# Kernel tuning notes

Hardware: AMD Instinct MI355X
Metric: run time of the kernel (lower is better)

Reference implementation:

```python
import jax, jax.numpy as jnp
import numpy as np

EMB = 2048
HD = 64            # head_dim
NH = 32            # n_heads
NKV = 8            # n_kv_groups
GS = NH // NKV     # group_size = 4
WIN = 128          # sliding_window
LAYER_IDX = 0      # even -> sliding-window mask active
ROPE_BASE = 10000.0
MAX_SEQ = 4096
YARN_ORIG = 1024.0
YARN_SCALE = 4.0
YARN_BETA_FAST = 32.0
YARN_BETA_SLOW = 1.0


def _rope_tables():
    # YaRN-adjusted RoPE tables, shape [MAX_SEQ, HD]
    freqs = 1.0 / ROPE_BASE ** (np.arange(0, HD, 2, dtype=np.float32) / HD)
    wave_len = 2.0 * np.pi / freqs
    low = YARN_ORIG / YARN_BETA_FAST
    high = YARN_ORIG / YARN_BETA_SLOW
    t = np.clip((wave_len - low) / (high - low), 0.0, 1.0)
    eff = freqs * (1.0 - t) + (freqs / YARN_SCALE) * t
    conc = 0.1 * np.log(YARN_SCALE) + 1.0
    ang = (np.arange(MAX_SEQ, dtype=np.float32)[:, None] * eff[None, :]) * conc
    ang = np.concatenate([ang, ang], axis=-1).astype(np.float32)
    return jnp.sin(ang), jnp.cos(ang)


def _apply_rope(x, sin, cos):
    # x: [B, H, S, D]; sin/cos: [B, S, D] -> broadcast over heads
    sin = sin[:, None, :, :]
    cos = cos[:, None, :, :]
    x1 = x[..., : HD // 2]
    x2 = x[..., HD // 2 :]
    rotated = jnp.concatenate([-x2, x1], axis=-1)
    return x * cos + rotated * sin


def setup_inputs() -> dict:
    key = jax.random.key(0)
    ks = jax.random.split(key, 8)
    B, S = 2, 2048
    s = 0.02
    x = jax.random.normal(ks[0], (B, S, EMB), dtype=jnp.float32)
    Wq = jax.random.normal(ks[1], (NH * HD, EMB), dtype=jnp.float32) * s
    Wk = jax.random.normal(ks[2], (NKV * HD, EMB), dtype=jnp.float32) * s
    Wv = jax.random.normal(ks[3], (NKV * HD, EMB), dtype=jnp.float32) * s
    Wo = jax.random.normal(ks[4], (EMB, NH * HD), dtype=jnp.float32) * s
    bq = jnp.zeros((NH * HD,), dtype=jnp.float32)
    bk = jnp.zeros((NKV * HD,), dtype=jnp.float32)
    bv = jnp.zeros((NKV * HD,), dtype=jnp.float32)
    bo = jnp.zeros((EMB,), dtype=jnp.float32)
    sinks = jax.random.normal(ks[5], (1, NH, 1, 1), dtype=jnp.float32)
    position_ids = jnp.arange(B * S, dtype=jnp.int64 if jax.config.jax_enable_x64 else jnp.int32).reshape(B, S)
    return {"x": x, "Wq": Wq, "bq": bq, "Wk": Wk, "bk": bk, "Wv": Wv, "bv": bv,
            "Wo": Wo, "bo": bo, "sinks": sinks, "position_ids": position_ids}


def reference(x, Wq, bq, Wk, bk, Wv, bv, Wo, bo, sinks, position_ids):
    B, S, _ = x.shape
    sin_t, cos_t = _rope_tables()
    sin = sin_t[position_ids]  # [B, S, HD]
    cos = cos_t[position_ids]

    Q = (x @ Wq.T + bq).reshape(B, S, NH, HD).transpose(0, 2, 1, 3)    # [B,NH,S,D]
    K = (x @ Wk.T + bk).reshape(B, S, NKV, HD).transpose(0, 2, 1, 3)   # [B,NKV,S,D]
    V = (x @ Wv.T + bv).reshape(B, S, NKV, HD).transpose(0, 2, 1, 3)

    Q = _apply_rope(Q, sin, cos)
    K = _apply_rope(K, sin, cos)

    # GQA without materializing repeated K/V: group query heads by kv group
    Qg = Q.reshape(B, NKV, GS, S, HD)
    scores = jnp.einsum('bgqsd,bgtd->bgqst', Qg, K) / np.sqrt(HD).astype(np.float32)

    i = jnp.arange(S)[:, None]
    j = jnp.arange(S)[None, :]
    allowed = (j <= i) & (j > i - WIN)
    scores = jnp.where(allowed, scores, -jnp.inf)

    # attention-sink logit prepended before softmax, then dropped
    sink = jnp.broadcast_to(sinks.reshape(1, NKV, GS, 1, 1), (B, NKV, GS, S, 1))
    full = jnp.concatenate([sink, scores], axis=-1)
    attn = jax.nn.softmax(full, axis=-1)[..., 1:]

    ctx = jnp.einsum('bgqst,bgtd->bgqsd', attn, V)
    ctx = ctx.reshape(B, NH, S, HD).transpose(0, 2, 1, 3).reshape(B, S, NH * HD)
    out = ctx @ Wo.T + bo
    return out
```

## Files before the change

kernel.cpp:

```cpp
#include <hip/hip_runtime.h>

typedef unsigned short u16;
typedef __bf16 bf16x8 __attribute__((ext_vector_type(8)));
typedef float f32x4 __attribute__((ext_vector_type(4)));
typedef unsigned short us8 __attribute__((ext_vector_type(8)));

__device__ inline u16 f2bf(float f) {
    union { float f; unsigned u; } v; v.f = f;
    unsigned r = v.u + 0x7FFFu + ((v.u >> 16) & 1u);
    return (u16)(r >> 16);
}
__device__ inline float bf2f(u16 h) {
    union { unsigned u; float f; } v; v.u = ((unsigned)h) << 16;
    return v.f;
}
__device__ inline f32x4 mfma16(bf16x8 a, bf16x8 b, f32x4 c) {
    return __builtin_amdgcn_mfma_f32_16x16x32_bf16(a, b, c, 0, 0, 0);
}
__device__ inline void gload_lds16(const u16* g, u16* l) {
    __builtin_amdgcn_global_load_lds(
        (const __attribute__((address_space(1))) void*)g,
        (__attribute__((address_space(3))) void*)l, 16, 0, 0);
}
union frag_cast { us8 u; bf16x8 b; };

__global__ __launch_bounds__(256)
void pack_all(const float* __restrict__ x,  const float* __restrict__ Wq,
              const float* __restrict__ Wk, const float* __restrict__ Wv,
              const float* __restrict__ Wo, const float* __restrict__ bq,
              const float* __restrict__ bk, const float* __restrict__ bv,
              u16* __restrict__ xb, u16* __restrict__ Wqkvb,
              u16* __restrict__ Wob, float* __restrict__ bqkv,
              float2* __restrict__ tab)
{
    int blk = blockIdx.x;
    if (blk >= 9217) {
        int idx = (blk - 9217) * 256 + threadIdx.x;
        int d = idx & 31, pos = idx >> 5;
        float ex = (float)d * (1.0f / 32.0f);
        float freq = powf(10000.0f, -ex);
        float wl = 6.2831853071795864f / freq;
        float tt = fminf(fmaxf((wl - 32.0f) * (1.0f / 992.0f), 0.0f), 1.0f);
        float eff = (freq * (1.0f - tt) + 0.25f * freq * tt) * 1.1386294361119891f;
        float ang = (float)pos * eff;
        tab[idx] = make_float2(cosf(ang), sinf(ang));
        return;
    }
    if (blk == 9216) {
        for (int k = threadIdx.x; k < 3072; k += 256) {
            float v;
            if (k < 2048) v = bq[k];
            else if (k < 2560) v = bk[k - 2048];
            else v = bv[k - 2560];
            bqkv[k] = v;
        }
        return;
    }
    const float* src; u16* dst; size_t off;
    if (blk < 4096)      { src = x;  dst = xb;                 off = (size_t)blk * 2048; }
    else if (blk < 6144) { src = Wq; dst = Wqkvb;              off = (size_t)(blk - 4096) * 2048; }
    else if (blk < 6656) { src = Wk; dst = Wqkvb + 4194304;    off = (size_t)(blk - 6144) * 2048; }
    else if (blk < 7168) { src = Wv; dst = Wqkvb + 5242880;    off = (size_t)(blk - 6656) * 2048; }
    else                 { src = Wo; dst = Wob;                off = (size_t)(blk - 7168) * 2048; }
    size_t i = off + (size_t)threadIdx.x * 8;
    float4 v0 = *(const float4*)(src + i);
    float4 v1 = *(const float4*)(src + i + 4);
    us8 w;
    w[0] = f2bf(v0.x); w[1] = f2bf(v0.y); w[2] = f2bf(v0.z); w[3] = f2bf(v0.w);
    w[4] = f2bf(v1.x); w[5] = f2bf(v1.y); w[6] = f2bf(v1.z); w[7] = f2bf(v1.w);
    *(us8*)(dst + i) = w;
}

template<int NBX, int OUT_BF16>
__global__ __launch_bounds__(256, 3)
void gemm_128(const u16* __restrict__ A, const u16* __restrict__ B,
              const float* __restrict__ bias, void* __restrict__ Yv,
              int M, int N, int K)
{
    __shared__ u16 lds[3 * 8192];

    const int tid = threadIdx.x;
    const int lane = tid & 63;
    const int w = tid >> 6;
    const int wr = w >> 1, wc = w & 1;
    const int wg = blockIdx.x;
    const int cpx = (NBX * 32) >> 3;
    const int swz = (wg & 7) * cpx + (wg >> 3);
    const int by = swz / NBX, bx = swz - by * NBX;
    const long m0 = (long)by * 128;
    const long n0 = (long)bx * 128;
    const int cc = lane & 15, qq = lane >> 4;
    const int csw = (qq ^ ((cc >> 1) & 3)) << 3;

    const int sr = lane >> 2;
    const int colsw = ((lane & 3) ^ ((lane >> 3) & 3)) << 3;
    const u16* gA0 = A + (m0 + w * 16 + sr) * (long)K + colsw;
    const u16* gA1 = gA0 + 64 * (long)K;
    const u16* gB0 = B + (n0 + w * 16 + sr) * (long)K + colsw;
    const u16* gB1 = gB0 + 64 * (long)K;

    const int NT = K >> 5;

    auto STAGE = [&](int k0, int bi) {
        u16* buf = &lds[bi * 8192];
        gload_lds16(gA0 + k0, buf + w * 512);
        gload_lds16(gA1 + k0, buf + (4 + w) * 512);
        gload_lds16(gB0 + k0, buf + (8 + w) * 512);
        gload_lds16(gB1 + k0, buf + (12 + w) * 512);
    };

    f32x4 acc[4][4];
#pragma unroll
    for (int i = 0; i < 4; i++)
#pragma unroll
        for (int j = 0; j < 4; j++) acc[i][j] = (f32x4){0.f, 0.f, 0.f, 0.f};

    STAGE(0, 0);
    int bR = 0;
    for (int t = 0; t < NT; ++t) {
        int bW = bR + 1; if (bW == 3) bW = 0;
        if (t + 1 < NT) {
            STAGE((t + 1) << 5, bW);
            asm volatile("s_waitcnt vmcnt(4)" ::: "memory");
        } else {
            asm volatile("s_waitcnt vmcnt(0)" ::: "memory");
        }
        __builtin_amdgcn_s_barrier();
        __builtin_amdgcn_sched_barrier(0);

        const u16* Ab = &lds[bR * 8192];
        bf16x8 af[4], bfr[4];
#pragma unroll
        for (int j = 0; j < 4; ++j)
            bfr[j] = *(const bf16x8*)&Ab[4096 + (wc * 64 + j * 16 + cc) * 32 + csw];
#pragma unroll
        for (int i = 0; i < 4; ++i)
            af[i] = *(const bf16x8*)&Ab[(wr * 64 + i * 16 + cc) * 32 + csw];

        __builtin_amdgcn_s_setprio(1);
#pragma unroll
        for (int i = 0; i < 4; ++i)
#pragma unroll
            for (int j = 0; j < 4; ++j)
                acc[i][j] = mfma16(af[i], bfr[j], acc[i][j]);
        __builtin_amdgcn_s_setprio(0);
        bR = bW;
    }

#pragma unroll
    for (int i = 0; i < 4; ++i) {
#pragma unroll
        for (int j = 0; j < 4; ++j) {
            long row = m0 + wr * 64 + i * 16 + qq * 4;
            long col = n0 + wc * 64 + j * 16 + cc;
            float bvv = bias[col];
#pragma unroll
            for (int r2 = 0; r2 < 4; ++r2) {
                float v = acc[i][j][r2] + bvv;
                if (OUT_BF16)
                    ((u16*)Yv)[(row + r2) * (long)N + col] = f2bf(v);
                else
                    ((float*)Yv)[(row + r2) * (long)N + col] = v;
            }
        }
    }
}

__global__ __launch_bounds__(256)
void v_transpose(const u16* __restrict__ Vt, u16* __restrict__ VbT)
{
    __shared__ u16 tile[64][66];
    int s0 = blockIdx.x * 64;
    int bkv = blockIdx.y;
    int b = bkv >> 3, kv = bkv & 7;
    int t = threadIdx.x;
#pragma unroll
    for (int it = 0; it < 16; ++it) {
        int idx = t + it * 256;
        int s = idx >> 6, d = idx & 63;
        tile[s][d] = Vt[((size_t)(b * 2048 + s0 + s)) * 3072 + 2560 + kv * 64 + d];
    }
    __syncthreads();
#pragma unroll
    for (int it = 0; it < 16; ++it) {
        int idx = t + it * 256;
        int d = idx >> 6, s = idx & 63;
        VbT[((size_t)(bkv * 64 + d)) * 2048 + s0 + s] = tile[s][d];
    }
}

__global__ __launch_bounds__(256, 2)
void attn_win2(const u16* __restrict__ QKVr, const u16* __restrict__ VbT,
               const float2* __restrict__ tab, const int* __restrict__ pid,
               const float* __restrict__ sinks, u16* __restrict__ Ctx)
{
    __shared__ u16 Ks[192 * 72];
    __shared__ u16 Vs[64 * 200];
    __shared__ u16 Pb[4 * 16 * 200];
    const int S = 2048;
    const int tid = threadIdx.x;
    const int lane = tid & 63;
    const int w = tid >> 6;
    const int cc = lane & 15, qq = lane >> 4;
    const int blk = blockIdx.x;
    const int qt = blk & 31;
    const int bkv = blk >> 5;
    const int b = bkv >> 3, kv = bkv & 7;
    const int q0 = qt * 64;
    const int ks0 = q0 - 128;
    const int h = kv * 4 + w;

    {
        const int kcol = 2048 + kv * 64;
#pragma unroll
        for (int it = 0; it < 3; ++it) {
            int c = tid + it * 256;
            int kk = c >> 2, dlo = (c & 3) << 3;
            int sk = ks0 + kk;
            us8 lo = {0, 0, 0, 0, 0, 0, 0, 0};
            us8 hi = {0, 0, 0, 0, 0, 0, 0, 0};
            if (sk >= 0) {
                size_t rowoff = (size_t)(b * S + sk) * 3072 + kcol;
                us8 li = *(const us8*)(QKVr + rowoff + dlo);
                us8 hiQ = *(const us8*)(QKVr + rowoff + dlo + 32);
                int pos = pid[b * S + sk];
                const float2* tp = tab + pos * 32 + dlo;
#pragma unroll
                for (int jj = 0; jj < 8; ++jj) {
                    float2 cs = tp[jj];
                    float x1 = bf2f(li[jj]), x2 = bf2f(hiQ[jj]);
                    lo[jj] = f2bf(x1 * cs.x - x2 * cs.y);
                    hi[jj] = f2bf(x2 * cs.x + x1 * cs.y);
                }
            }
            *(us8*)&Ks[kk * 72 + dlo] = lo;
            *(us8*)&Ks[kk * 72 + dlo + 32] = hi;
        }
    }
    const u16* VtBase = VbT + (size_t)bkv * 64 * S;
#pragma unroll
    for (int it = 0; it < 6; ++it) {
        int c = tid + it * 256;
        int d = c / 24, kc = c % 24;
        int kk0 = kc << 3;
        int sk = ks0 + kk0;
        us8 v = {0, 0, 0, 0, 0, 0, 0, 0};
        if (sk >= 0) v = *(const us8*)(VtBase + (size_t)d * S + sk);
        *(us8*)&Vs[d * 200 + kk0] = v;
    }
    __syncthreads();

    const float sinkv = sinks[h];
    u16* Pw = &Pb[w * 3200];

    for (int i = 0; i < 4; ++i) {
        int m = b * S + q0 + i * 16 + cc;
        const u16* Qrow = QKVr + (size_t)m * 3072 + h * 64;
        us8 qlo = *(const us8*)(Qrow + qq * 8);
        us8 qhi = *(const us8*)(Qrow + 32 + qq * 8);
        int pos = pid[m];
        const float2* tp = tab + pos * 32 + qq * 8;
        frag_cast a0, a1;
#pragma unroll
        for (int jj = 0; jj < 8; ++jj) {
            float2 cs = tp[jj];
            float x1 = bf2f(qlo[jj]), x2 = bf2f(qhi[jj]);
            a0.u[jj] = f2bf(x1 * cs.x - x2 * cs.y);
            a1.u[jj] = f2bf(x2 * cs.x + x1 * cs.y);
        }
        bf16x8 aq0 = a0.b, aq1 = a1.b;

        f32x4 sc[12];
#pragma unroll
        for (int j = 0; j < 12; j++) sc[j] = (f32x4){0.f, 0.f, 0.f, 0.f};
#pragma unroll
        for (int j = 0; j < 12; j++) {
            bf16x8 b0 = *(const bf16x8*)&Ks[(j * 16 + cc) * 72 + qq * 8];
            bf16x8 b1 = *(const bf16x8*)&Ks[(j * 16 + cc) * 72 + 32 + qq * 8];
            sc[j] = mfma16(aq0, b0, sc[j]);
            sc[j] = mfma16(aq1, b1, sc[j]);
        }

#pragma unroll
        for (int r = 0; r < 4; ++r) {
            int qi = i * 16 + qq * 4 + r;
            float sval[12];
            float mx = -3.0e38f;
#pragma unroll
            for (int j = 0; j < 12; j++) {
                int kk = j * 16 + cc;
                float s = sc[j][r] * 0.125f;
                bool ok = (kk > qi) && (kk <= qi + 128) && (ks0 + kk >= 0);
                s = ok ? s : -3.0e38f;
                sval[j] = s;
                mx = fmaxf(mx, s);
            }
#pragma unroll
            for (int off = 1; off < 16; off <<= 1) mx = fmaxf(mx, __shfl_xor(mx, off));
            mx = fmaxf(mx, sinkv);
            float sum = 0.f;
#pragma unroll
            for (int j = 0; j < 12; j++) {
                float p = __expf(sval[j] - mx);
                sval[j] = p;
                sum += p;
            }
#pragma unroll
            for (int off = 1; off < 16; off <<= 1) sum += __shfl_xor(sum, off);
            float rden = 1.0f / (sum + __expf(sinkv - mx));
#pragma unroll
            for (int j = 0; j < 12; j++)
                Pw[(qq * 4 + r) * 200 + j * 16 + cc] = f2bf(sval[j] * rden);
        }

        f32x4 o[4];
#pragma unroll
        for (int jt = 0; jt < 4; jt++) o[jt] = (f32x4){0.f, 0.f, 0.f, 0.f};
#pragma unroll
        for (int ks = 0; ks < 6; ks++) {
            bf16x8 ap = *(const bf16x8*)&Pw[cc * 200 + ks * 32 + qq * 8];
#pragma unroll
            for (int jt = 0; jt < 4; jt++) {
                bf16x8 bv = *(const bf16x8*)&Vs[(jt * 16 + cc) * 200 + ks * 32 + qq * 8];
                o[jt] = mfma16(ap, bv, o[jt]);
            }
        }
#pragma unroll
        for (int jt = 0; jt < 4; jt++) {
#pragma unroll
            for (int r = 0; r < 4; r++) {
                size_t off = ((size_t)(b * S + q0 + i * 16 + qq * 4 + r)) * 2048
                           + h * 64 + jt * 16 + cc;
                Ctx[off] = f2bf(o[jt][r]);
            }
        }
    }
}

extern "C" void kernel_launch(void* const* d_in, const int* in_sizes, int n_in,
                              void* d_out, int out_size, void* d_ws, size_t ws_size,
                              hipStream_t stream)
{
    const float* x    = (const float*)d_in[0];
    const float* Wq   = (const float*)d_in[1];
    const float* bq   = (const float*)d_in[2];
    const float* Wk   = (const float*)d_in[3];
    const float* bk   = (const float*)d_in[4];
    const float* Wv   = (const float*)d_in[5];
    const float* bv   = (const float*)d_in[6];
    const float* Wo   = (const float*)d_in[7];
    const float* bo   = (const float*)d_in[8];
    const float* sinks = (const float*)d_in[9];
    const int*   pid  = (const int*)d_in[10];
    float* out = (float*)d_out;

    char*  ws    = (char*)d_ws;
    u16*   Wqkvb = (u16*)ws;
    u16*   Wob   = (u16*)(ws + 12582912);
    u16*   xb    = (u16*)(ws + 20971520);
    u16*   Ctx   = xb;
    u16*   QKVr  = (u16*)(ws + 37748736);
    u16*   VbT   = (u16*)(ws + 62914560);
    float* bqkv  = (float*)(ws + 67108864);
    float2* tab  = (float2*)(ws + 67121152);

    pack_all<<<9729, 256, 0, stream>>>(x, Wq, Wk, Wv, Wo, bq, bk, bv,
                                       xb, Wqkvb, Wob, bqkv, tab);

    gemm_128<24, 1><<<768, 256, 0, stream>>>(xb, Wqkvb, bqkv, QKVr,
                                             4096, 3072, 2048);

    v_transpose<<<dim3(32, 16), 256, 0, stream>>>(QKVr, VbT);

    attn_win2<<<512, 256, 0, stream>>>(QKVr, VbT, tab, pid, sinks, Ctx);

    gemm_128<16, 0><<<512, 256, 0, stream>>>(Ctx, Wob, bo, out,
                                             4096, 2048, 2048);
}
```

Measured before the change: 263.6 us.

## Replace 128x128 GEMM with 256-row, 512-thread, double-buffered split-K-stage kernel

Both projection GEMMs move to a new kernel with 8 waves per block, a 256-row M tile and a wider N tile (192 for QKV, 128 for the output projection). Each iteration covers a 64-wide K step split into two 32-wide half stages, with the prefetch of the next half issued between the LDS fragment reads and the MFMA work. This doubles the LDS buffers and is meant to raise operand reuse per load and overlap global loads with compute. The costs are fewer blocks (256 per GEMM), so wave-level parallelism drops, plus higher register and LDS use per block and hand-tuned vmcnt counts that must match the issued loads exactly.

```diff
diff --git a/kernel.cpp b/kernel.cpp
--- a/kernel.cpp
+++ b/kernel.cpp
@@ -71,92 +71,143 @@
     *(us8*)(dst + i) = w;
 }
 
-template<int NBX, int OUT_BF16>
-__global__ __launch_bounds__(256, 3)
-void gemm_128(const u16* __restrict__ A, const u16* __restrict__ B,
-              const float* __restrict__ bias, void* __restrict__ Yv,
-              int M, int N, int K)
+template<int WNF, int VC1, int OUT_BF16>
+__global__ __launch_bounds__(512, 2)
+void gemm_dp(const u16* __restrict__ A, const u16* __restrict__ B,
+             const float* __restrict__ bias, void* __restrict__ Yv,
+             int M, int N, int K)
 {
-    __shared__ u16 lds[3 * 8192];
+    constexpr int BN = 32 * WNF;
+    constexpr int BSL = BN * 32;
+    constexpr int ABUF = 16384;
+    constexpr int BUFU = ABUF + 2 * BSL;
+    __shared__ u16 lds[2 * BUFU];
 
     const int tid = threadIdx.x;
     const int lane = tid & 63;
     const int w = tid >> 6;
     const int wr = w >> 1, wc = w & 1;
     const int wg = blockIdx.x;
-    const int cpx = (NBX * 32) >> 3;
-    const int swz = (wg & 7) * cpx + (wg >> 3);
-    const int by = swz / NBX, bx = swz - by * NBX;
-    const long m0 = (long)by * 128;
-    const long n0 = (long)bx * 128;
+    const int swz = (wg & 7) * 32 + (wg >> 3);
+    const int by = swz >> 4, bx = swz & 15;
+    const long m0 = (long)by * 256;
+    const long n0 = (long)bx * BN;
     const int cc = lane & 15, qq = lane >> 4;
     const int csw = (qq ^ ((cc >> 1) & 3)) << 3;
 
     const int sr = lane >> 2;
     const int colsw = ((lane & 3) ^ ((lane >> 3) & 3)) << 3;
-    const u16* gA0 = A + (m0 + w * 16 + sr) * (long)K + colsw;
-    const u16* gA1 = gA0 + 64 * (long)K;
-    const u16* gB0 = B + (n0 + w * 16 + sr) * (long)K + colsw;
-    const u16* gB1 = gB0 + 64 * (long)K;
-
-    const int NT = K >> 5;
-
-    auto STAGE = [&](int k0, int bi) {
-        u16* buf = &lds[bi * 8192];
-        gload_lds16(gA0 + k0, buf + w * 512);
-        gload_lds16(gA1 + k0, buf + (4 + w) * 512);
-        gload_lds16(gB0 + k0, buf + (8 + w) * 512);
-        gload_lds16(gB1 + k0, buf + (12 + w) * 512);
+    const u16* Ag = A + (m0 + sr) * (long)K + colsw;
+    const u16* Bg = B + (n0 + sr) * (long)K + colsw;
+
+    const int NT = K >> 6;
+
+    auto STAGE0 = [&](int u) {
+        u16* buf = &lds[(u & 1) * BUFU];
+        const long k0 = (long)u * 64;
+        gload_lds16(Ag + (size_t)(w * 16) * K + k0,        buf + (w * 16) * 32);
+        gload_lds16(Ag + (size_t)(128 + w * 16) * K + k0,  buf + (128 + w * 16) * 32);
+        gload_lds16(Bg + (size_t)(w * 16) * K + k0,        buf + ABUF + (w * 16) * 32);
+        if (WNF == 6) {
+            if (w < 4)
+                gload_lds16(Bg + (size_t)(128 + w * 16) * K + k0,
+                            buf + ABUF + (128 + w * 16) * 32);
+            else
+                gload_lds16(Bg + (size_t)((w - 4) * 16) * K + k0 + 32,
+                            buf + ABUF + BSL + ((w - 4) * 16) * 32);
+        }
     };
-
-    f32x4 acc[4][4];
-#pragma unroll
-    for (int i = 0; i < 4; i++)
-#pragma unroll
-        for (int j = 0; j < 4; j++) acc[i][j] = (f32x4){0.f, 0.f, 0.f, 0.f};
-
-    STAGE(0, 0);
-    int bR = 0;
+    auto STAGE1 = [&](int u) {
+        u16* buf = &lds[(u & 1) * BUFU];
+        const long k0 = (long)u * 64 + 32;
+        gload_lds16(Ag + (size_t)(w * 16) * K + k0,        buf + 8192 + (w * 16) * 32);
+        gload_lds16(Ag + (size_t)(128 + w * 16) * K + k0,  buf + 8192 + (128 + w * 16) * 32);
+        if (WNF == 6)
+            gload_lds16(Bg + (size_t)((w + 4) * 16) * K + k0,
+                        buf + ABUF + BSL + ((w + 4) * 16) * 32);
+        else
+            gload_lds16(Bg + (size_t)(w * 16) * K + k0,
+                        buf + ABUF + BSL + (w * 16) * 32);
+    };
+
+    f32x4 acc[4][WNF];
+#pragma unroll
+    for (int m = 0; m < 4; ++m)
+#pragma unroll
+        for (int n = 0; n < WNF; ++n) acc[m][n] = (f32x4){0.f, 0.f, 0.f, 0.f};
+
+    STAGE0(0);
+    STAGE1(0);
+
     for (int t = 0; t < NT; ++t) {
-        int bW = bR + 1; if (bW == 3) bW = 0;
+        const u16* buf = &lds[(t & 1) * BUFU];
+
+        asm volatile("s_waitcnt vmcnt(3)" ::: "memory");
+        __builtin_amdgcn_s_barrier();
+        __builtin_amdgcn_sched_barrier(0);
+        {
+            const u16* Ab = buf;
+            const u16* Bb = buf + ABUF;
+            bf16x8 af[4], bfr[WNF];
+#pragma unroll
+            for (int n = 0; n < WNF; ++n)
+                bfr[n] = *(const bf16x8*)&Bb[(wc * (16 * WNF) + n * 16 + cc) * 32 + csw];
+#pragma unroll
+            for (int m = 0; m < 4; ++m)
+                af[m] = *(const bf16x8*)&Ab[(wr * 64 + m * 16 + cc) * 32 + csw];
+            if (t + 1 < NT) STAGE0(t + 1);
+            __builtin_amdgcn_sched_barrier(0);
+            __builtin_amdgcn_s_setprio(1);
+#pragma unroll
+            for (int m = 0; m < 4; ++m)
+#pragma unroll
+                for (int n = 0; n < WNF; ++n)
+                    acc[m][n] = mfma16(af[m], bfr[n], acc[m][n]);
+            __builtin_amdgcn_s_setprio(0);
+            __builtin_amdgcn_sched_barrier(0);
+        }
+
         if (t + 1 < NT) {
-            STAGE((t + 1) << 5, bW);
-            asm volatile("s_waitcnt vmcnt(4)" ::: "memory");
+            if (VC1 == 4) asm volatile("s_waitcnt vmcnt(4)" ::: "memory");
+            else          asm volatile("s_waitcnt vmcnt(3)" ::: "memory");
         } else {
             asm volatile("s_waitcnt vmcnt(0)" ::: "memory");
         }
         __builtin_amdgcn_s_barrier();
         __builtin_amdgcn_sched_barrier(0);
-
-        const u16* Ab = &lds[bR * 8192];
-        bf16x8 af[4], bfr[4];
-#pragma unroll
-        for (int j = 0; j < 4; ++j)
-            bfr[j] = *(const bf16x8*)&Ab[4096 + (wc * 64 + j * 16 + cc) * 32 + csw];
-#pragma unroll
-        for (int i = 0; i < 4; ++i)
-            af[i] = *(const bf16x8*)&Ab[(wr * 64 + i * 16 + cc) * 32 + csw];
-
-        __builtin_amdgcn_s_setprio(1);
-#pragma unroll
-        for (int i = 0; i < 4; ++i)
-#pragma unroll
-            for (int j = 0; j < 4; ++j)
-                acc[i][j] = mfma16(af[i], bfr[j], acc[i][j]);
-        __builtin_amdgcn_s_setprio(0);
-        bR = bW;
-    }
-
-#pragma unroll
-    for (int i = 0; i < 4; ++i) {
-#pragma unroll
-        for (int j = 0; j < 4; ++j) {
-            long row = m0 + wr * 64 + i * 16 + qq * 4;
-            long col = n0 + wc * 64 + j * 16 + cc;
+        {
+            const u16* Ab = buf + 8192;
+            const u16* Bb = buf + ABUF + BSL;
+            bf16x8 af[4], bfr[WNF];
+#pragma unroll
+            for (int n = 0; n < WNF; ++n)
+                bfr[n] = *(const bf16x8*)&Bb[(wc * (16 * WNF) + n * 16 + cc) * 32 + csw];
+#pragma unroll
+            for (int m = 0; m < 4; ++m)
+                af[m] = *(const bf16x8*)&Ab[(wr * 64 + m * 16 + cc) * 32 + csw];
+            if (t + 1 < NT) STAGE1(t + 1);
+            __builtin_amdgcn_sched_barrier(0);
+            __builtin_amdgcn_s_setprio(1);
+#pragma unroll
+            for (int m = 0; m < 4; ++m)
+#pragma unroll
+                for (int n = 0; n < WNF; ++n)
+                    acc[m][n] = mfma16(af[m], bfr[n], acc[m][n]);
+            __builtin_amdgcn_s_setprio(0);
+            __builtin_amdgcn_sched_barrier(0);
+        }
+    }
+
+#pragma unroll
+    for (int m = 0; m < 4; ++m) {
+#pragma unroll
+        for (int n = 0; n < WNF; ++n) {
+            long row = m0 + wr * 64 + m * 16 + qq * 4;
+            long col = n0 + wc * (16 * WNF) + n * 16 + cc;
             float bvv = bias[col];
 #pragma unroll
             for (int r2 = 0; r2 < 4; ++r2) {
-                float v = acc[i][j][r2] + bvv;
+                float v = acc[m][n][r2] + bvv;
                 if (OUT_BF16)
                     ((u16*)Yv)[(row + r2) * (long)N + col] = f2bf(v);
                 else
@@ -367,13 +418,13 @@
     pack_all<<<9729, 256, 0, stream>>>(x, Wq, Wk, Wv, Wo, bq, bk, bv,
                                        xb, Wqkvb, Wob, bqkv, tab);
 
-    gemm_128<24, 1><<<768, 256, 0, stream>>>(xb, Wqkvb, bqkv, QKVr,
-                                             4096, 3072, 2048);
+    gemm_dp<6, 4, 1><<<256, 512, 0, stream>>>(xb, Wqkvb, bqkv, QKVr,
+                                              4096, 3072, 2048);
 
     v_transpose<<<dim3(32, 16), 256, 0, stream>>>(QKVr, VbT);
 
     attn_win2<<<512, 256, 0, stream>>>(QKVr, VbT, tab, pid, sinks, Ctx);
 
-    gemm_128<16, 0><<<512, 256, 0, stream>>>(Ctx, Wob, bo, out,
-                                             4096, 2048, 2048);
-}
+    gemm_dp<4, 3, 0><<<256, 512, 0, stream>>>(Ctx, Wob, bo, out,
+                                              4096, 2048, 2048);
+}
```

After: 251.1 us. -4.8%, faster.
